# Optimization experiments

Measured on AMD Instinct MI355X. Metric: run time of the kernel, lower is better.

## Reference

```python
import jax, jax.numpy as jnp
import numpy as np

TEMPERATURE = 0.07
B, D = 8192, 256

def _l2norm(x, axis=-1, eps=1e-12):
    # matches torch F.normalize(p=2): x / max(||x||, eps)
    n = jnp.sqrt(jnp.sum(x * x, axis=axis, keepdims=True))
    return x / jnp.maximum(n, eps)

def setup_inputs() -> dict:
    key = jax.random.key(0)
    k1, k2, k3 = jax.random.split(key, 3)
    return {
        "h_emb": jax.random.normal(k1, (B, D), dtype=jnp.float32),
        "r_emb": jax.random.normal(k2, (B, D), dtype=jnp.float32),
        "t_emb": jax.random.normal(k3, (B, D), dtype=jnp.float32),
    }

def reference(h_emb, r_emb, t_emb):
    # query = normalize(h + r); positives/negatives = normalize(t)
    q = _l2norm(h_emb + r_emb, axis=1)          # [B, D]
    t = _l2norm(t_emb, axis=1)                  # [B, D]
    # Dense in-batch similarity. The original builds logits = [pos, off-diag negs];
    # since the diagonal of sim IS the positive similarity, cross-entropy with
    # label 0 equals logsumexp over the full row minus the diagonal entry.
    sim = jnp.einsum('bd,nd->bn', q, t) / TEMPERATURE   # [B, B]
    pos = jnp.diagonal(sim)                              # [B]
    loss = jnp.mean(jax.nn.logsumexp(sim, axis=1) - pos)
    return loss
```

## Files before the change

### kernel.cpp

```cpp
#include <hip/hip_runtime.h>
#include <hip/hip_bf16.h>

#define B_DIM 8192
#define D_DIM 256
#define GRID_GEMM 256
#define NT 16

constexpr float INV_T = 14.285714285714286f;

typedef __bf16 bf16x8 __attribute__((ext_vector_type(8)));
typedef float  f32x4  __attribute__((ext_vector_type(4)));

#define GLOBAL_U32(p) ((const __attribute__((address_space(1))) unsigned int*)(p))
#define LDS_U32(p)    ((__attribute__((address_space(3))) unsigned int*)(p))

#define WAITCNT_VM8 0x0F78

__device__ inline unsigned short f2bf(float f) {
    union { float f; unsigned u; } x; x.f = f;
    unsigned r = x.u + 0x7fffu + ((x.u >> 16) & 1u);
    return (unsigned short)(r >> 16);
}

__global__ __launch_bounds__(256) void norm_kernel(
    const float* __restrict__ h, const float* __restrict__ r,
    const float* __restrict__ t,
    unsigned short* __restrict__ qws, unsigned short* __restrict__ tws,
    float* __restrict__ rowsum, float* __restrict__ diagsum, int* __restrict__ ticket)
{
    if (blockIdx.x == 0) {
        float4* rs4 = (float4*)rowsum;
#pragma unroll
        for (int i = 0; i < 8; ++i)
            rs4[threadIdx.x * 8 + i] = make_float4(0.f, 0.f, 0.f, 0.f);
        if (threadIdx.x == 0) { *diagsum = 0.f; *ticket = 0; }
    }

    const int wave = threadIdx.x >> 6;
    const int lane = threadIdx.x & 63;
    const int wg   = blockIdx.x * 4 + wave;

    const int kst  = lane >> 3;
    const int krun = (lane >> 1) & 3;
    const int sub8 = lane & 1;

#pragma unroll
    for (int i = 0; i < 2; ++i) {
        const int row = wg * 2 + i;
        {
            float4 a = ((const float4*)h)[row * 64 + lane];
            float4 b = ((const float4*)r)[row * 64 + lane];
            float4 v = make_float4(a.x + b.x, a.y + b.y, a.z + b.z, a.w + b.w);
            float s = v.x * v.x + v.y * v.y + v.z * v.z + v.w * v.w;
#pragma unroll
            for (int off = 32; off; off >>= 1) s += __shfl_xor(s, off, 64);
            float scale = INV_T / fmaxf(sqrtf(s), 1e-12f);
            ushort4 o;
            o.x = f2bf(v.x * scale); o.y = f2bf(v.y * scale);
            o.z = f2bf(v.z * scale); o.w = f2bf(v.w * scale);
            size_t slot16 = ((size_t)((row >> 4) * 8 + kst) * 64
                             + (size_t)(krun * 16 + (row & 15)));
            *(ushort4*)((unsigned char*)qws + slot16 * 16 + sub8 * 8) = o;
        }
        {
            float4 v = ((const float4*)t)[row * 64 + lane];
            float s = v.x * v.x + v.y * v.y + v.z * v.z + v.w * v.w;
#pragma unroll
            for (int off = 32; off; off >>= 1) s += __shfl_xor(s, off, 64);
            float scale = 1.0f / fmaxf(sqrtf(s), 1e-12f);
            ushort4 o;
            o.x = f2bf(v.x * scale); o.y = f2bf(v.y * scale);
            o.z = f2bf(v.z * scale); o.w = f2bf(v.w * scale);
            size_t slot16 = ((size_t)((row >> 4) * 8 + kst) * 64
                             + (size_t)(krun * 16 + (row & 31 & 15)));
            slot16 = ((size_t)((row >> 4) * 8 + kst) * 64
                      + (size_t)(krun * 16 + (row & 15)));
            *(ushort4*)((unsigned char*)tws + slot16 * 16 + sub8 * 8) = o;
        }
    }
}

__global__ __launch_bounds__(512, 2) void gemm_lse_kernel(
    const unsigned char* __restrict__ qws, const unsigned char* __restrict__ tws,
    float* __restrict__ rowsum, float* __restrict__ diagsum,
    int* __restrict__ ticket, float* __restrict__ out)
{
    __shared__ __align__(16) unsigned char ldsB[8][16384];
    __shared__ float wred[8];
    __shared__ int lastflag;

    const int tid  = threadIdx.x;
    const int lane = tid & 63;
    const int w    = tid >> 6;
    const int l15  = lane & 15;
    const int hi4  = lane >> 4;

    const int cc   = blockIdx.x & 15;
    const int rb   = blockIdx.x >> 4;
    const int row0 = rb * 512 + w * 64;
    const int col0 = cc * 512;
    const int tile0 = cc * 16;

#define STAGE(st, bufi)                                                      \
    {                                                                        \
        const unsigned char* gs = tws + (size_t)(tile0 + (st)) * 16384;      \
        _Pragma("unroll")                                                    \
        for (int it = 0; it < 2; ++it)                                       \
            __builtin_amdgcn_global_load_lds(                                \
                GLOBAL_U32(gs + (it * 512 + tid) * 16),                      \
                LDS_U32(&ldsB[bufi][(it * 512 + tid) * 16]), 16, 0, 0);      \
    }

    STAGE(0, 0); STAGE(1, 1);
    STAGE(2, 2); STAGE(3, 3);
    STAGE(4, 4); STAGE(5, 5);

    bf16x8 a[4][8];
    {
        const unsigned char* abase = qws + (size_t)row0 * 512 + lane * 16;
#pragma unroll
        for (int r = 0; r < 4; ++r)
#pragma unroll
            for (int kst = 0; kst < 8; ++kst)
                a[r][kst] = *(const bf16x8*)(abase + r * 8192 + kst * 1024);
    }

    float rowacc[16] = {};
    float diagacc = 0.f;

#define PROCESS_TILE(t)                                                      \
    {                                                                        \
        const unsigned char* bbuf = ldsB[(t) & 7] + lane * 16;               \
        f32x4 acc[4][2] = {};                                                \
        _Pragma("unroll")                                                    \
        for (int kst = 0; kst < 8; ++kst) {                                  \
            bf16x8 b0 = *(const bf16x8*)(bbuf + kst * 1024);                 \
            bf16x8 b1 = *(const bf16x8*)(bbuf + 8192 + kst * 1024);         \
            _Pragma("unroll")                                                \
            for (int r = 0; r < 4; ++r) {                                    \
                acc[r][0] = __builtin_amdgcn_mfma_f32_16x16x32_bf16(         \
                                a[r][kst], b0, acc[r][0], 0, 0, 0);          \
                acc[r][1] = __builtin_amdgcn_mfma_f32_16x16x32_bf16(         \
                                a[r][kst], b1, acc[r][1], 0, 0, 0);          \
            }                                                                \
        }                                                                    \
        _Pragma("unroll")                                                    \
        for (int r = 0; r < 4; ++r)                                          \
            _Pragma("unroll")                                                \
            for (int g2 = 0; g2 < 4; ++g2)                                   \
                rowacc[r * 4 + g2] += __expf(acc[r][0][g2] - INV_T)          \
                                    + __expf(acc[r][1][g2] - INV_T);         \
        const int c0t = col0 + (t) * 32;                                     \
        if (c0t == row0) {                                                   \
            _Pragma("unroll")                                                \
            for (int g2 = 0; g2 < 4; ++g2)                                   \
                if (l15 == hi4 * 4 + g2)                                     \
                    diagacc += acc[0][0][g2] + acc[1][1][g2];                \
        }                                                                    \
        if (c0t == row0 + 32) {                                              \
            _Pragma("unroll")                                                \
            for (int g2 = 0; g2 < 4; ++g2)                                   \
                if (l15 == hi4 * 4 + g2)                                     \
                    diagacc += acc[2][0][g2] + acc[3][1][g2];                \
        }                                                                    \
    }

    for (int r = 0; r < 8; ++r) {
        __builtin_amdgcn_s_waitcnt(WAITCNT_VM8);
        __builtin_amdgcn_s_barrier();
        const int p = (r + 3 < 8) ? r + 3 : 7;
        STAGE(2 * p,     (2 * r + 6) & 7);
        STAGE(2 * p + 1, (2 * r + 7) & 7);
        PROCESS_TILE(2 * r);
        PROCESS_TILE(2 * r + 1);
    }

#pragma unroll
    for (int rr = 0; rr < 16; ++rr) {
        float s = rowacc[rr];
        s += __shfl_xor(s, 1, 64);
        s += __shfl_xor(s, 2, 64);
        s += __shfl_xor(s, 4, 64);
        s += __shfl_xor(s, 8, 64);
        if (l15 == 0) {
            int grow = row0 + (rr >> 2) * 16 + hi4 * 4 + (rr & 3);
            atomicAdd(&rowsum[grow], s);
        }
    }

    float dsum = diagacc;
#pragma unroll
    for (int off = 32; off; off >>= 1) dsum += __shfl_xor(dsum, off, 64);
    if (lane == 0 && dsum != 0.f) atomicAdd(diagsum, dsum);

    __syncthreads();
    if (tid == 0) {
        __threadfence();
        int old = __hip_atomic_fetch_add(ticket, 1, __ATOMIC_ACQ_REL,
                                         __HIP_MEMORY_SCOPE_AGENT);
        lastflag = (old == GRID_GEMM - 1);
    }
    __syncthreads();
    if (!lastflag) return;

    float lsum = 0.f;
    for (int rr = tid; rr < B_DIM; rr += 512) {
        float rs = __hip_atomic_load(&rowsum[rr], __ATOMIC_RELAXED,
                                     __HIP_MEMORY_SCOPE_AGENT);
        lsum += __logf(rs);
    }
#pragma unroll
    for (int off = 32; off; off >>= 1) lsum += __shfl_xor(lsum, off, 64);
    if (lane == 0) wred[w] = lsum;
    __syncthreads();
    if (tid == 0) {
        float total = wred[0] + wred[1] + wred[2] + wred[3]
                    + wred[4] + wred[5] + wred[6] + wred[7]
                    + (float)B_DIM * INV_T
                    - __hip_atomic_load(diagsum, __ATOMIC_RELAXED,
                                        __HIP_MEMORY_SCOPE_AGENT);
        out[0] = total / (float)B_DIM;
    }
}

extern "C" void kernel_launch(void* const* d_in, const int* in_sizes, int n_in,
                              void* d_out, int out_size, void* d_ws, size_t ws_size,
                              hipStream_t stream)
{
    const float* h = (const float*)d_in[0];
    const float* r = (const float*)d_in[1];
    const float* t = (const float*)d_in[2];

    unsigned char* ws = (unsigned char*)d_ws;
    unsigned short* qws = (unsigned short*)ws;
    unsigned short* tws = (unsigned short*)(ws + 4u * 1024 * 1024);
    float* rowsum  = (float*)(ws + 8u * 1024 * 1024);
    float* diagsum = (float*)(ws + 8u * 1024 * 1024 + 32u * 1024);
    int*   ticket  = (int*)  (ws + 8u * 1024 * 1024 + 32u * 1024 + 16);

    norm_kernel<<<1024, 256, 0, stream>>>(h, r, t, qws, tws, rowsum, diagsum, ticket);
    gemm_lse_kernel<<<GRID_GEMM, 512, 0, stream>>>(
        (const unsigned char*)qws, (const unsigned char*)tws,
        rowsum, diagsum, ticket, (float*)d_out);
}
```

Measured before the change: 119.9 us.

## Overlap exp epilogue with next tile's MFMAs and fold log2e into query scale

Splits per-tile processing into an MFMA phase and an exp/diagonal epilogue, then software-pipelines them with two accumulator sets so one tile's exponentials are issued while the next tile's MFMAs run. The query normalization scale is changed to (1/T)*log2(e), so the epilogue can call exp2f directly without an extra multiply, and the diagonal sum is rescaled by ln2 to compensate. This hides transcendental latency behind matrix work but doubles the live accumulator registers. That could add spills or lower occupancy under the 512-thread, 2-block launch bound.

```diff
diff --git a/kernel.cpp b/kernel.cpp
--- a/kernel.cpp
+++ b/kernel.cpp
@@ -6,7 +6,9 @@
 #define GRID_GEMM 256
 #define NT 16
 
-constexpr float INV_T = 14.285714285714286f;
+constexpr float INV_T  = 14.285714285714286f;
+constexpr float QSCALE = 20.609929155556605f;
+constexpr float LN2F   = 0.6931471805599453f;
 
 typedef __bf16 bf16x8 __attribute__((ext_vector_type(8)));
 typedef float  f32x4  __attribute__((ext_vector_type(4)));
@@ -47,6 +49,8 @@
 #pragma unroll
     for (int i = 0; i < 2; ++i) {
         const int row = wg * 2 + i;
+        const size_t slot16 = ((size_t)((row >> 4) * 8 + kst) * 64
+                               + (size_t)(krun * 16 + (row & 15)));
         {
             float4 a = ((const float4*)h)[row * 64 + lane];
             float4 b = ((const float4*)r)[row * 64 + lane];
@@ -54,12 +58,10 @@
             float s = v.x * v.x + v.y * v.y + v.z * v.z + v.w * v.w;
 #pragma unroll
             for (int off = 32; off; off >>= 1) s += __shfl_xor(s, off, 64);
-            float scale = INV_T / fmaxf(sqrtf(s), 1e-12f);
+            float scale = QSCALE / fmaxf(sqrtf(s), 1e-12f);
             ushort4 o;
             o.x = f2bf(v.x * scale); o.y = f2bf(v.y * scale);
             o.z = f2bf(v.z * scale); o.w = f2bf(v.w * scale);
-            size_t slot16 = ((size_t)((row >> 4) * 8 + kst) * 64
-                             + (size_t)(krun * 16 + (row & 15)));
             *(ushort4*)((unsigned char*)qws + slot16 * 16 + sub8 * 8) = o;
         }
         {
@@ -71,10 +73,6 @@
             ushort4 o;
             o.x = f2bf(v.x * scale); o.y = f2bf(v.y * scale);
             o.z = f2bf(v.z * scale); o.w = f2bf(v.w * scale);
-            size_t slot16 = ((size_t)((row >> 4) * 8 + kst) * 64
-                             + (size_t)(krun * 16 + (row & 31 & 15)));
-            slot16 = ((size_t)((row >> 4) * 8 + kst) * 64
-                      + (size_t)(krun * 16 + (row & 15)));
             *(ushort4*)((unsigned char*)tws + slot16 * 16 + sub8 * 8) = o;
         }
     }
@@ -127,41 +125,50 @@
 
     float rowacc[16] = {};
     float diagacc = 0.f;
-
-#define PROCESS_TILE(t)                                                      \
+    f32x4 accE[4][2], accO[4][2];
+
+#define MFMA_TILE(t, ACC)                                                    \
     {                                                                        \
         const unsigned char* bbuf = ldsB[(t) & 7] + lane * 16;               \
-        f32x4 acc[4][2] = {};                                                \
+        _Pragma("unroll")                                                    \
+        for (int r4 = 0; r4 < 4; ++r4)                                       \
+            _Pragma("unroll")                                                \
+            for (int cg = 0; cg < 2; ++cg)                                   \
+                ACC[r4][cg] = (f32x4){};                                     \
         _Pragma("unroll")                                                    \
         for (int kst = 0; kst < 8; ++kst) {                                  \
             bf16x8 b0 = *(const bf16x8*)(bbuf + kst * 1024);                 \
-            bf16x8 b1 = *(const bf16x8*)(bbuf + 8192 + kst * 1024);         \
-            _Pragma("unroll")                                                \
-            for (int r = 0; r < 4; ++r) {                                    \
-                acc[r][0] = __builtin_amdgcn_mfma_f32_16x16x32_bf16(         \
-                                a[r][kst], b0, acc[r][0], 0, 0, 0);          \
-                acc[r][1] = __builtin_amdgcn_mfma_f32_16x16x32_bf16(         \
-                                a[r][kst], b1, acc[r][1], 0, 0, 0);          \
+            bf16x8 b1 = *(const bf16x8*)(bbuf + 8192 + kst * 1024);          \
+            _Pragma("unroll")                                                \
+            for (int r4 = 0; r4 < 4; ++r4) {                                 \
+                ACC[r4][0] = __builtin_amdgcn_mfma_f32_16x16x32_bf16(        \
+                                 a[r4][kst], b0, ACC[r4][0], 0, 0, 0);       \
+                ACC[r4][1] = __builtin_amdgcn_mfma_f32_16x16x32_bf16(        \
+                                 a[r4][kst], b1, ACC[r4][1], 0, 0, 0);       \
             }                                                                \
         }                                                                    \
-        _Pragma("unroll")                                                    \
-        for (int r = 0; r < 4; ++r)                                          \
+    }
+
+#define EPI_DIAG(t, ACC)                                                     \
+    {                                                                        \
+        _Pragma("unroll")                                                    \
+        for (int r4 = 0; r4 < 4; ++r4)                                       \
             _Pragma("unroll")                                                \
             for (int g2 = 0; g2 < 4; ++g2)                                   \
-                rowacc[r * 4 + g2] += __expf(acc[r][0][g2] - INV_T)          \
-                                    + __expf(acc[r][1][g2] - INV_T);         \
+                rowacc[r4 * 4 + g2] += exp2f(ACC[r4][0][g2] - QSCALE)        \
+                                     + exp2f(ACC[r4][1][g2] - QSCALE);       \
         const int c0t = col0 + (t) * 32;                                     \
         if (c0t == row0) {                                                   \
             _Pragma("unroll")                                                \
             for (int g2 = 0; g2 < 4; ++g2)                                   \
                 if (l15 == hi4 * 4 + g2)                                     \
-                    diagacc += acc[0][0][g2] + acc[1][1][g2];                \
+                    diagacc += ACC[0][0][g2] + ACC[1][1][g2];                \
         }                                                                    \
         if (c0t == row0 + 32) {                                              \
             _Pragma("unroll")                                                \
             for (int g2 = 0; g2 < 4; ++g2)                                   \
                 if (l15 == hi4 * 4 + g2)                                     \
-                    diagacc += acc[2][0][g2] + acc[3][1][g2];                \
+                    diagacc += ACC[2][0][g2] + ACC[3][1][g2];                \
         }                                                                    \
     }
 
@@ -171,9 +178,13 @@
         const int p = (r + 3 < 8) ? r + 3 : 7;
         STAGE(2 * p,     (2 * r + 6) & 7);
         STAGE(2 * p + 1, (2 * r + 7) & 7);
-        PROCESS_TILE(2 * r);
-        PROCESS_TILE(2 * r + 1);
-    }
+
+        MFMA_TILE(2 * r, accE);
+        if (r > 0) EPI_DIAG(2 * r - 1, accO);
+        MFMA_TILE(2 * r + 1, accO);
+        EPI_DIAG(2 * r, accE);
+    }
+    EPI_DIAG(15, accO);
 
 #pragma unroll
     for (int rr = 0; rr < 16; ++rr) {
@@ -188,7 +199,7 @@
         }
     }
 
-    float dsum = diagacc;
+    float dsum = diagacc * LN2F;
 #pragma unroll
     for (int off = 32; off; off >>= 1) dsum += __shfl_xor(dsum, off, 64);
     if (lane == 0 && dsum != 0.f) atomicAdd(diagsum, dsum);
```

Result: slower. 137.4 us (+14.5%).
